# Performance work log

Hardware: AMD Instinct MI355X
Metric: run time of the kernel (lower is better)

Reference implementation:

```python
import jax, jax.numpy as jnp
import numpy as np

NB = 4
QN = -(2 ** (NB - 1))   # -8
QP = 2 ** (NB - 1) - 1  # 7
EPS = 1e-5


def _grad_scale(x, g):
    # forward: x, backward: grad * g (LSQ gradient scaling)
    return x * g + jax.lax.stop_gradient(x - x * g)


def _round_pass(x):
    # round with straight-through estimator
    return x + jax.lax.stop_gradient(jnp.round(x) - x)


def _lsq(v, alpha, qn, qp):
    # LSQ fake quantize-dequantize with learnable step size alpha
    g = 1.0 / np.sqrt(v.size * qp)
    a = _grad_scale(alpha, g)
    return _round_pass(jnp.clip(v / a, qn, qp)) * a


def _bn(x, g, b, m, v):
    # eval-mode BatchNorm2d over channel dim of NCHW
    s = (g * jax.lax.rsqrt(v + EPS))[None, :, None, None]
    return (x - m[None, :, None, None]) * s + b[None, :, None, None]


def _conv(x, w, stride, pad, groups):
    return jax.lax.conv_general_dilated(
        x, w, (stride, stride), pad,
        dimension_numbers=('NCHW', 'OIHW', 'NCHW'),
        feature_group_count=groups)


def setup_inputs() -> dict:
    key = jax.random.key(0)
    ks = jax.random.split(key, 4)
    inp, oup, hid = 96, 96, 576
    B, H, W = 32, 28, 28
    d = {}
    d['x'] = jax.random.normal(ks[0], (B, inp, H, W), jnp.float32)
    d['w1'] = jax.random.normal(ks[1], (hid, inp, 1, 1), jnp.float32) * 0.1
    d['w2'] = jax.random.normal(ks[2], (hid, 1, 3, 3), jnp.float32) * 0.1
    d['w3'] = jax.random.normal(ks[3], (oup, hid, 1, 1), jnp.float32) * 0.1
    for i, c in zip((1, 2, 3), (hid, hid, oup)):
        d[f'aw{i}'] = jnp.full((1,), 0.05, jnp.float32)  # weight step size
        d[f'ax{i}'] = jnp.full((1,), 0.5, jnp.float32)   # activation step size
        d[f'g{i}'] = jnp.ones((c,), jnp.float32)
        d[f'b{i}'] = jnp.zeros((c,), jnp.float32)
        d[f'm{i}'] = jnp.zeros((c,), jnp.float32)
        d[f'v{i}'] = jnp.ones((c,), jnp.float32)
    return d


def reference(x, w1, w2, w3, aw1, ax1, g1, b1, m1, v1,
              aw2, ax2, g2, b2, m2, v2, aw3, ax3, g3, b3, m3, v3):
    hid = w1.shape[0]
    # 1x1 expand conv (LSQ on activation and weight)
    h = _conv(_lsq(x, ax1, QN, QP), _lsq(w1, aw1, QN, QP), 1, [(0, 0), (0, 0)], 1)
    h = jnp.clip(_bn(h, g1, b1, m1, v1), 0.0, 6.0)
    # 3x3 depthwise conv, stride 1
    h = _conv(_lsq(h, ax2, QN, QP), _lsq(w2, aw2, QN, QP), 1, [(1, 1), (1, 1)], hid)
    h = jnp.clip(_bn(h, g2, b2, m2, v2), 0.0, 6.0)
    # 1x1 project conv
    h = _conv(_lsq(h, ax3, QN, QP), _lsq(w3, aw3, QN, QP), 1, [(0, 0), (0, 0)], 1)
    h = _bn(h, g3, b3, m3, v3)
    # identity residual (stride==1 and inp==oup)
    return x + h
```

## Files before the change

### kernel.cpp

```cpp
#include <hip/hip_runtime.h>

#define EPSF 1e-5f

typedef int    int4v   __attribute__((ext_vector_type(4)));
typedef float  float4v __attribute__((ext_vector_type(4)));

#define W1P_OFF  0
#define W3P_OFF  55296
#define W2D_OFF  110592
#define S1B1_OFF 202752
#define S2B2_OFF 207360
#define S3B3_OFF 211968

#define H1S 296
#define H2S 300

__device__ __forceinline__ float lsq_q(float v, float a) {
    float t = v / a;
    t = fminf(fmaxf(t, -8.0f), 7.0f);
    return rintf(t);
}

__device__ __forceinline__ long q8pack_w(const float* w, int base, const int* idx, float a) {
    unsigned long long v = 0;
    #pragma unroll
    for (int j = 0; j < 8; ++j) {
        int q = (int)lsq_q(w[base + idx[j]], a);
        v |= (unsigned long long)(q & 255) << (8 * j);
    }
    return (long)v;
}

__global__ __launch_bounds__(128)
void prep_w(const float* __restrict__ w1, const float* __restrict__ w2,
            const float* __restrict__ w3,
            const float* aw1, const float* ax1, const float* ax2,
            const float* aw2, const float* ax3, const float* aw3,
            const float* __restrict__ g1, const float* __restrict__ b1,
            const float* __restrict__ m1, const float* __restrict__ v1,
            const float* __restrict__ g2, const float* __restrict__ b2,
            const float* __restrict__ m2, const float* __restrict__ v2,
            const float* __restrict__ g3, const float* __restrict__ b3,
            const float* __restrict__ m3, const float* __restrict__ v3,
            long* __restrict__ w1p, long* __restrict__ w3p,
            long* __restrict__ w2d,
            float* __restrict__ s1b1, float* __restrict__ s2b2,
            float* __restrict__ s3b3) {
    int id = blockIdx.x * 128 + threadIdx.x;
    const int lin[8] = {0, 1, 2, 3, 4, 5, 6, 7};
    const int prm[8] = {0, 2, 4, 6, 1, 3, 5, 7};
    if (id < 6912) {
        int l = id & 63, t = id >> 6;
        int kc = t % 3, ct = t / 3;
        int co = ct * 16 + (l & 15);
        int ci0 = kc * 32 + (l >> 4) * 8;
        w1p[id] = q8pack_w(w1, co * 96 + ci0, lin, aw1[0]);
    } else if (id < 13824) {
        int i = id - 6912;
        int l = i & 63, t = i >> 6;
        int kc = t % 18, ct = t / 18;
        int co = ct * 16 + (l & 15);
        int ci0 = kc * 32 + (l >> 4) * 8;
        w3p[i] = q8pack_w(w3, co * 576 + ci0, prm, aw3[0]);
    } else if (id < 25344) {
        int i = id - 13824;
        int l = i & 63, t = i >> 6;
        int kc = t % 5, ct = t / 5;
        int quad = l >> 4, m = l & 15;
        int tap = kc * 2 + (quad >> 1);
        unsigned long long v = 0;
        if (tap <= 8) {
            int mh = m - (quad & 1) * 8;
            if (mh >= 0 && mh < 8) {
                int j = (mh >> 1) | ((mh & 1) << 2);
                int q = (int)lsq_q(w2[(ct * 16 + m) * 9 + tap], aw2[0]);
                v = (unsigned long long)(unsigned)(q & 255) << (8 * j);
            }
        }
        w2d[i] = (long)v;
    } else if (id < 25920) {
        int c = id - 25344;
        float s = g1[c] / sqrtf(v1[c] + EPSF);
        float A = aw1[0] * ax1[0];
        float inv = 1.0f / ax2[0];
        s1b1[c] = A * s * inv;
        s1b1[576 + c] = (b1[c] - m1[c] * s) * inv;
    } else if (id < 26496) {
        int c = id - 25920;
        float s = g2[c] / sqrtf(v2[c] + EPSF);
        float A = ax2[0] * aw2[0];
        float inv = 1.0f / ax3[0];
        s2b2[c] = A * s * inv;
        s2b2[576 + c] = (b2[c] - m2[c] * s) * inv;
    } else if (id < 26592) {
        int c = id - 26496;
        float s = g3[c] / sqrtf(v3[c] + EPSF);
        float A = ax3[0] * aw3[0];
        s3b3[c] = A * s;
        s3b3[96 + c] = b3[c] - m3[c] * s;
    }
}

__global__ __launch_bounds__(448, 4)
void fused_k(const float* __restrict__ x, const long* __restrict__ w1p,
             const long* __restrict__ w2d, const long* __restrict__ w3p,
             const float* __restrict__ ax1,
             const float* __restrict__ s1b1, const float* __restrict__ s2b2,
             const float* __restrict__ s3b3, float* __restrict__ out) {
    __shared__ __align__(16) signed char h1[120 * H1S];
    __shared__ __align__(16) signed char h2[57 * H2S];
    const int tid = threadIdx.x;
    const int w = tid >> 6, l = tid & 63;
    const int quad = l >> 4, c16 = l & 15;
    const int qh = quad >> 1, ql = quad & 1;
    const int b = blockIdx.x;
    const int r0 = blockIdx.y * 2;

    for (int i = tid; i < 120 * H1S / 16; i += 448)
        ((int4v*)h1)[i] = (int4v){0, 0, 0, 0};
    __syncthreads();

    {
        const int lp = w * 16 + c16;
        const int row = lp / 28, col = lp - (lp / 28) * 28;
        const int img_row = r0 - 1 + row;
        const bool valid = (unsigned)img_row < 28u;
        const int p = min(max(img_row, 0), 27) * 28 + col;
        const float inv1 = 1.0f / ax1[0];

        long bfr[3];
        #pragma unroll
        for (int kc = 0; kc < 3; ++kc) {
            const float* xs = x + (b * 96 + kc * 32 + quad * 8) * 784 + p;
            unsigned long long v = 0;
            #pragma unroll
            for (int j = 0; j < 8; ++j) {
                float t = xs[j * 784] * inv1;
                t = fminf(fmaxf(t, -8.0f), 7.0f);
                int q = (int)rintf(t);
                v |= (unsigned long long)(q & 255) << (8 * j);
            }
            bfr[kc] = (long)v;
        }
        const int pos_h = row * 30 + col + 1;
        #pragma unroll 4
        for (int ct = 0; ct < 36; ++ct) {
            int4v acc; acc[0] = 0; acc[1] = 0; acc[2] = 0; acc[3] = 0;
            #pragma unroll
            for (int kc = 0; kc < 3; ++kc)
                acc = __builtin_amdgcn_mfma_i32_16x16x32_i8(
                    w1p[(ct * 3 + kc) * 64 + l], bfr[kc], acc, 0, 0, 0);
            const int co0 = ct * 16 + quad * 4;
            float4v S = *(const float4v*)(s1b1 + co0);
            float4v B = *(const float4v*)(s1b1 + 576 + co0);
            int pk = 0;
            #pragma unroll
            for (int r = 0; r < 4; ++r) {
                float t = fmaf((float)acc[r], S[r], B[r]);
                t = fminf(fmaxf(t, 0.0f), 7.0f);
                pk |= ((int)rintf(t)) << (4 * r);
            }
            if (valid)
                *(unsigned short*)(h1 + pos_h * H1S + (co0 >> 1)) = (unsigned short)pk;
        }
    }
    __syncthreads();

    for (int t = w; t < 144; t += 7) {
        const int pt = t / 36, ct = t - (t / 36) * 36;
        const int pos = pt * 16 + c16;
        const int posc = min(pos, 55);
        const int row_in = posc / 28, col = posc - (posc / 28) * 28;
        const int choff = ct * 8 + ql * 4;
        int4v acc; acc[0] = 0; acc[1] = 0; acc[2] = 0; acc[3] = 0;
        #pragma unroll
        for (int kc = 0; kc < 5; ++kc) {
            int tap = kc * 2 + qh;
            tap = min(tap, 8);
            const int dh = tap / 3 - 1, dc = tap - (tap / 3) * 3 - 1;
            const int pos_h = (row_in + 1 + dh) * 30 + (col + 1 + dc);
            const unsigned v = *(const unsigned*)(h1 + pos_h * H1S + choff);
            const unsigned lo = v & 0x0F0F0F0Fu;
            const unsigned hi = (v >> 4) & 0x0F0F0F0Fu;
            const long bf = (long)(((unsigned long long)hi << 32) | lo);
            acc = __builtin_amdgcn_mfma_i32_16x16x32_i8(
                w2d[(ct * 5 + kc) * 64 + l], bf, acc, 0, 0, 0);
        }
        if (pos < 56) {
            const int c0 = ct * 16 + quad * 4;
            float4v S = *(const float4v*)(s2b2 + c0);
            float4v B = *(const float4v*)(s2b2 + 576 + c0);
            int pk = 0;
            #pragma unroll
            for (int r = 0; r < 4; ++r) {
                float tt = fmaf((float)acc[r], S[r], B[r]);
                tt = fminf(fmaxf(tt, 0.0f), 7.0f);
                pk |= ((int)rintf(tt)) << (4 * r);
            }
            *(unsigned short*)(h2 + pos * H2S + (c0 >> 1)) = (unsigned short)pk;
        }
    }
    __syncthreads();

    for (int t = w; t < 24; t += 7) {
        const int nt = t / 6, ct = t - (t / 6) * 6;
        int4v acc; acc[0] = 0; acc[1] = 0; acc[2] = 0; acc[3] = 0;
        const int pr = min(nt * 16 + c16, 56);
        const signed char* arow = h2 + pr * H2S + quad * 4;
        #pragma unroll 6
        for (int kc = 0; kc < 18; ++kc) {
            const unsigned v = *(const unsigned*)(arow + kc * 16);
            const unsigned lo = v & 0x0F0F0F0Fu;
            const unsigned hi = (v >> 4) & 0x0F0F0F0Fu;
            acc = __builtin_amdgcn_mfma_i32_16x16x32_i8(
                (long)(((unsigned long long)hi << 32) | lo),
                w3p[(ct * 18 + kc) * 64 + l], acc, 0, 0, 0);
        }
        const int nloc = nt * 16 + quad * 4;
        if (nloc < 56) {
            const int co = ct * 16 + c16;
            const float S = s3b3[co], Bv = s3b3[96 + co];
            const int off = (b * 96 + co) * 784 + r0 * 28 + nloc;
            const float4v xr = *(const float4v*)(x + off);
            float4v o;
            #pragma unroll
            for (int r = 0; r < 4; ++r)
                o[r] = fmaf((float)acc[r], S, Bv) + xr[r];
            *(float4v*)(out + off) = o;
        }
    }
}

extern "C" void kernel_launch(void* const* d_in, const int* in_sizes, int n_in,
                              void* d_out, int out_size, void* d_ws, size_t ws_size,
                              hipStream_t stream) {
    const float* x   = (const float*)d_in[0];
    const float* w1  = (const float*)d_in[1];
    const float* w2  = (const float*)d_in[2];
    const float* w3  = (const float*)d_in[3];
    const float* aw1 = (const float*)d_in[4];
    const float* ax1 = (const float*)d_in[5];
    const float* g1  = (const float*)d_in[6];
    const float* b1  = (const float*)d_in[7];
    const float* m1  = (const float*)d_in[8];
    const float* v1  = (const float*)d_in[9];
    const float* aw2 = (const float*)d_in[10];
    const float* ax2 = (const float*)d_in[11];
    const float* g2  = (const float*)d_in[12];
    const float* b2  = (const float*)d_in[13];
    const float* m2  = (const float*)d_in[14];
    const float* v2  = (const float*)d_in[15];
    const float* aw3 = (const float*)d_in[16];
    const float* ax3 = (const float*)d_in[17];
    const float* g3  = (const float*)d_in[18];
    const float* b3  = (const float*)d_in[19];
    const float* m3  = (const float*)d_in[20];
    const float* v3  = (const float*)d_in[21];

    char* ws = (char*)d_ws;
    long* w1p = (long*)(ws + W1P_OFF);
    long* w3p = (long*)(ws + W3P_OFF);
    long* w2d = (long*)(ws + W2D_OFF);
    float* s1b1 = (float*)(ws + S1B1_OFF);
    float* s2b2 = (float*)(ws + S2B2_OFF);
    float* s3b3 = (float*)(ws + S3B3_OFF);

    float* out = (float*)d_out;

    prep_w<<<208, 128, 0, stream>>>(w1, w2, w3, aw1, ax1, ax2, aw2, ax3, aw3,
                                    g1, b1, m1, v1, g2, b2, m2, v2, g3, b3, m3, v3,
                                    w1p, w3p, w2d, s1b1, s2b2, s3b3);
    dim3 grid(32, 14);
    fused_k<<<grid, 448, 0, stream>>>(x, w1p, w2d, w3p, ax1, s1b1, s2b2, s3b3, out);
}
```

Measured before the change: 145.4 us.

## Shrink fused block tile to one output row for more blocks and occupancy

Each block now computes one output row instead of two: the grid doubles to 32x28, blocks use 384 threads (6 waves), and shared buffers shrink. The aim is more resident blocks per CU and less wasted padding work in the depthwise and project stages. In exchange, the halo rows of the expand conv are recomputed more often (3 input rows per 1 output row instead of 4 per 2), and the weights are reloaded by twice as many blocks.

```diff
diff --git a/kernel.cpp b/kernel.cpp
--- a/kernel.cpp
+++ b/kernel.cpp
@@ -13,7 +13,7 @@
 #define S3B3_OFF 211968
 
 #define H1S 296
-#define H2S 300
+#define H2S 304
 
 __device__ __forceinline__ float lsq_q(float v, float a) {
     float t = v / a;
@@ -101,30 +101,30 @@
     }
 }
 
-__global__ __launch_bounds__(448, 4)
+__global__ __launch_bounds__(384, 6)
 void fused_k(const float* __restrict__ x, const long* __restrict__ w1p,
              const long* __restrict__ w2d, const long* __restrict__ w3p,
              const float* __restrict__ ax1,
              const float* __restrict__ s1b1, const float* __restrict__ s2b2,
              const float* __restrict__ s3b3, float* __restrict__ out) {
-    __shared__ __align__(16) signed char h1[120 * H1S];
-    __shared__ __align__(16) signed char h2[57 * H2S];
+    __shared__ __align__(16) signed char h1[90 * H1S];
+    __shared__ __align__(16) signed char h2[32 * H2S];
     const int tid = threadIdx.x;
     const int w = tid >> 6, l = tid & 63;
     const int quad = l >> 4, c16 = l & 15;
     const int qh = quad >> 1, ql = quad & 1;
     const int b = blockIdx.x;
-    const int r0 = blockIdx.y * 2;
-
-    for (int i = tid; i < 120 * H1S / 16; i += 448)
+    const int r = blockIdx.y;
+
+    for (int i = tid; i < 90 * H1S / 16; i += 384)
         ((int4v*)h1)[i] = (int4v){0, 0, 0, 0};
     __syncthreads();
 
     {
         const int lp = w * 16 + c16;
         const int row = lp / 28, col = lp - (lp / 28) * 28;
-        const int img_row = r0 - 1 + row;
-        const bool valid = (unsigned)img_row < 28u;
+        const int img_row = r - 1 + row;
+        const bool valid = (lp < 84) && ((unsigned)img_row < 28u);
         const int p = min(max(img_row, 0), 27) * 28 + col;
         const float inv1 = 1.0f / ax1[0];
 
@@ -155,10 +155,10 @@
             float4v B = *(const float4v*)(s1b1 + 576 + co0);
             int pk = 0;
             #pragma unroll
-            for (int r = 0; r < 4; ++r) {
-                float t = fmaf((float)acc[r], S[r], B[r]);
+            for (int r2 = 0; r2 < 4; ++r2) {
+                float t = fmaf((float)acc[r2], S[r2], B[r2]);
                 t = fminf(fmaxf(t, 0.0f), 7.0f);
-                pk |= ((int)rintf(t)) << (4 * r);
+                pk |= ((int)rintf(t)) << (4 * r2);
             }
             if (valid)
                 *(unsigned short*)(h1 + pos_h * H1S + (co0 >> 1)) = (unsigned short)pk;
@@ -166,11 +166,10 @@
     }
     __syncthreads();
 
-    for (int t = w; t < 144; t += 7) {
+    for (int t = w; t < 72; t += 6) {
         const int pt = t / 36, ct = t - (t / 36) * 36;
         const int pos = pt * 16 + c16;
-        const int posc = min(pos, 55);
-        const int row_in = posc / 28, col = posc - (posc / 28) * 28;
+        const int col = min(pos, 27);
         const int choff = ct * 8 + ql * 4;
         int4v acc; acc[0] = 0; acc[1] = 0; acc[2] = 0; acc[3] = 0;
         #pragma unroll
@@ -178,7 +177,7 @@
             int tap = kc * 2 + qh;
             tap = min(tap, 8);
             const int dh = tap / 3 - 1, dc = tap - (tap / 3) * 3 - 1;
-            const int pos_h = (row_in + 1 + dh) * 30 + (col + 1 + dc);
+            const int pos_h = (1 + dh) * 30 + (col + 1 + dc);
             const unsigned v = *(const unsigned*)(h1 + pos_h * H1S + choff);
             const unsigned lo = v & 0x0F0F0F0Fu;
             const unsigned hi = (v >> 4) & 0x0F0F0F0Fu;
@@ -186,27 +185,26 @@
             acc = __builtin_amdgcn_mfma_i32_16x16x32_i8(
                 w2d[(ct * 5 + kc) * 64 + l], bf, acc, 0, 0, 0);
         }
-        if (pos < 56) {
+        if (pos < 28) {
             const int c0 = ct * 16 + quad * 4;
             float4v S = *(const float4v*)(s2b2 + c0);
             float4v B = *(const float4v*)(s2b2 + 576 + c0);
             int pk = 0;
             #pragma unroll
-            for (int r = 0; r < 4; ++r) {
-                float tt = fmaf((float)acc[r], S[r], B[r]);
+            for (int r2 = 0; r2 < 4; ++r2) {
+                float tt = fmaf((float)acc[r2], S[r2], B[r2]);
                 tt = fminf(fmaxf(tt, 0.0f), 7.0f);
-                pk |= ((int)rintf(tt)) << (4 * r);
+                pk |= ((int)rintf(tt)) << (4 * r2);
             }
             *(unsigned short*)(h2 + pos * H2S + (c0 >> 1)) = (unsigned short)pk;
         }
     }
     __syncthreads();
 
-    for (int t = w; t < 24; t += 7) {
+    for (int t = w; t < 12; t += 6) {
         const int nt = t / 6, ct = t - (t / 6) * 6;
         int4v acc; acc[0] = 0; acc[1] = 0; acc[2] = 0; acc[3] = 0;
-        const int pr = min(nt * 16 + c16, 56);
-        const signed char* arow = h2 + pr * H2S + quad * 4;
+        const signed char* arow = h2 + (nt * 16 + c16) * H2S + quad * 4;
         #pragma unroll 6
         for (int kc = 0; kc < 18; ++kc) {
             const unsigned v = *(const unsigned*)(arow + kc * 16);
@@ -217,15 +215,15 @@
                 w3p[(ct * 18 + kc) * 64 + l], acc, 0, 0, 0);
         }
         const int nloc = nt * 16 + quad * 4;
-        if (nloc < 56) {
+        if (nloc < 28) {
             const int co = ct * 16 + c16;
             const float S = s3b3[co], Bv = s3b3[96 + co];
-            const int off = (b * 96 + co) * 784 + r0 * 28 + nloc;
+            const int off = (b * 96 + co) * 784 + r * 28 + nloc;
             const float4v xr = *(const float4v*)(x + off);
             float4v o;
             #pragma unroll
-            for (int r = 0; r < 4; ++r)
-                o[r] = fmaf((float)acc[r], S, Bv) + xr[r];
+            for (int r2 = 0; r2 < 4; ++r2)
+                o[r2] = fmaf((float)acc[r2], S, Bv) + xr[r2];
             *(float4v*)(out + off) = o;
         }
     }
@@ -270,6 +268,6 @@
     prep_w<<<208, 128, 0, stream>>>(w1, w2, w3, aw1, ax1, ax2, aw2, ax3, aw3,
                                     g1, b1, m1, v1, g2, b2, m2, v2, g3, b3, m3, v3,
                                     w1p, w3p, w2d, s1b1, s2b2, s3b3);
-    dim3 grid(32, 14);
-    fused_k<<<grid, 448, 0, stream>>>(x, w1p, w2d, w3p, ax1, s1b1, s2b2, s3b3, out);
-}
+    dim3 grid(32, 28);
+    fused_k<<<grid, 384, 0, stream>>>(x, w1p, w2d, w3p, ax1, s1b1, s2b2, s3b3, out);
+}
```

New measurement: 165.9 us. 14.1% more time.
